# Kernel tuning notes

Hardware: AMD Instinct MI355X
Metric: run time of the kernel (lower is better)

Reference implementation:

```python
import jax, jax.numpy as jnp
import numpy as np

N, F_IN, H1, C1, C2, Q, E = 50000, 256, 4, 32, 128, 768, 800000
NEG_SLOPE = 0.2


def gat_layer(x, src, dst, W, a_src, a_dst, bias, heads, ch, num_nodes):
    # x: [N, F]; W: [F, heads*ch]; a_src/a_dst: [heads, ch]
    xw = (x @ W).reshape(num_nodes, heads, ch)
    alpha_s = jnp.sum(xw * a_src, axis=-1)  # [N, heads]
    alpha_d = jnp.sum(xw * a_dst, axis=-1)  # [N, heads]
    e = jax.nn.leaky_relu(alpha_s[src] + alpha_d[dst], NEG_SLOPE)  # [E, heads]
    # segment softmax over destination nodes (every node has a self-loop)
    m = jax.ops.segment_max(e, dst, num_segments=num_nodes)
    e = jnp.exp(e - m[dst])
    denom = jax.ops.segment_sum(e, dst, num_segments=num_nodes)
    alpha = e / (denom[dst] + 1e-16)  # [E, heads]
    msg = alpha[:, :, None] * xw[src]  # [E, heads, ch]
    out = jax.ops.segment_sum(msg, dst, num_segments=num_nodes)
    return out.reshape(num_nodes, heads * ch) + bias


def setup_inputs() -> dict:
    key = jax.random.key(0)
    ks = jax.random.split(key, 16)
    s = lambda fan_in: 1.0 / np.sqrt(fan_in)
    return {
        "entity_features": jax.random.normal(ks[0], (N, F_IN), jnp.float32),
        "edge_index": jax.random.randint(ks[1], (2, E), 0, N, jnp.int32),
        "question_embedding": jax.random.normal(ks[2], (Q,), jnp.float32),
        "question_entity_mask": jax.random.randint(ks[3], (N,), 0, 2, jnp.int32),
        "place_entity_mask": jax.random.randint(ks[4], (N,), 0, 2, jnp.int32),
        "W1": jax.random.normal(ks[5], (F_IN, H1 * C1), jnp.float32) * s(F_IN),
        "att_src1": jax.random.normal(ks[6], (H1, C1), jnp.float32) * s(C1),
        "att_dst1": jax.random.normal(ks[7], (H1, C1), jnp.float32) * s(C1),
        "b1": jnp.zeros((H1 * C1,), jnp.float32),
        "W2": jax.random.normal(ks[8], (H1 * C1, C2), jnp.float32) * s(H1 * C1),
        "att_src2": jax.random.normal(ks[9], (1, C2), jnp.float32) * s(C2),
        "att_dst2": jax.random.normal(ks[10], (1, C2), jnp.float32) * s(C2),
        "b2": jnp.zeros((C2,), jnp.float32),
        "Wq": jax.random.normal(ks[11], (C2 + Q, 1), jnp.float32) * s(C2 + Q),
        "bq": jnp.zeros((1,), jnp.float32),
    }


def reference(entity_features, edge_index, question_embedding, question_entity_mask,
              place_entity_mask, W1, att_src1, att_dst1, b1, W2, att_src2, att_dst2, b2, Wq, bq):
    # add self-loops (PyG GATConv default add_self_loops=True)
    loops = jnp.arange(N, dtype=edge_index.dtype)
    src = jnp.concatenate([edge_index[0], loops])
    dst = jnp.concatenate([edge_index[1], loops])

    x = gat_layer(entity_features, src, dst, W1, att_src1, att_dst1, b1, H1, C1, N)
    x = jax.nn.elu(x)  # dropout is identity in eval
    ents = gat_layer(x, src, dst, W2, att_src2, att_dst2, b2, 1, C2, N)
    ents = jax.nn.elu(ents)  # [N, C2]

    q = jnp.broadcast_to(question_embedding[None, :], (N, Q))
    combined = jnp.concatenate([ents, q], axis=-1)  # [N, C2+Q]
    logits = (combined @ Wq + bq)[:, 0]  # [N]
    logits = logits + (question_entity_mask.astype(jnp.float32) - 1.0) * 1e9
    attn = jax.nn.softmax(logits, axis=0)  # [N]
    pooled = jnp.sum(attn[:, None] * ents, axis=0)  # [C2]
    return pooled, ents, attn
```

## Files before the change

### kernel.cpp

```cpp
#include <hip/hip_runtime.h>
#include <hip/hip_fp16.h>
#include <math.h>

#define N_NODES 50000
#define F_IN    256
#define H1      4
#define C1      32
#define HC      128
#define C2      128
#define QDIM    768
#define NE      800000
#define NB_SCAN 196
#define NB_POOL 512


__device__ __forceinline__ void atomicMaxFloat(float* addr, float val) {
    if (val >= 0.f)
        atomicMax(reinterpret_cast<int*>(addr), __float_as_int(val));
    else
        atomicMin(reinterpret_cast<unsigned int*>(addr), __float_as_uint(val));
}


__global__ void init_scal_kernel(float* scal) {
    scal[1] = -INFINITY;
    scal[2] = 0.f;
}

__global__ void qdot_kernel(const float* __restrict__ q, const float* __restrict__ Wq,
                            const float* __restrict__ bq, float* scal) {
    __shared__ float sm[256];
    float acc = 0.f;
    for (int i = threadIdx.x; i < QDIM; i += 256) acc += q[i] * Wq[C2 + i];
    sm[threadIdx.x] = acc;
    __syncthreads();
    for (int o = 128; o > 0; o >>= 1) {
        if (threadIdx.x < o) sm[threadIdx.x] += sm[threadIdx.x + o];
        __syncthreads();
    }
    if (threadIdx.x == 0) scal[0] = sm[0] + bq[0];
}


__global__ void hist_kernel(const int* __restrict__ ei, int* __restrict__ deg) {
    int e = blockIdx.x * blockDim.x + threadIdx.x;
    if (e >= NE) return;
    atomicAdd(&deg[ei[NE + e]], 1);
}

__global__ void scan1_kernel(const int* __restrict__ deg, int* __restrict__ incl,
                             int* __restrict__ bsum) {
    __shared__ int sm[256];
    int i = blockIdx.x * 256 + threadIdx.x;
    int v = (i < N_NODES) ? deg[i] : 0;
    sm[threadIdx.x] = v;
    __syncthreads();
    for (int o = 1; o < 256; o <<= 1) {
        int t = (threadIdx.x >= o) ? sm[threadIdx.x - o] : 0;
        __syncthreads();
        sm[threadIdx.x] += t;
        __syncthreads();
    }
    if (i < N_NODES) incl[i] = sm[threadIdx.x];
    if (threadIdx.x == 255) bsum[blockIdx.x] = sm[255];
}

__global__ void scan2_kernel(int* __restrict__ bsum) {
    __shared__ int sm[256];
    int v = (threadIdx.x < NB_SCAN) ? bsum[threadIdx.x] : 0;
    sm[threadIdx.x] = v;
    __syncthreads();
    for (int o = 1; o < 256; o <<= 1) {
        int t = (threadIdx.x >= o) ? sm[threadIdx.x - o] : 0;
        __syncthreads();
        sm[threadIdx.x] += t;
        __syncthreads();
    }
    if (threadIdx.x < NB_SCAN) bsum[threadIdx.x] = sm[threadIdx.x] - v;
}

__global__ void scan3_kernel(const int* __restrict__ deg, const int* __restrict__ incl,
                             const int* __restrict__ bsum, int* __restrict__ rowptr,
                             int* __restrict__ cursor) {
    int i = blockIdx.x * 256 + threadIdx.x;
    if (i >= N_NODES) return;
    int excl = incl[i] - deg[i] + bsum[i >> 8];
    rowptr[i] = excl;
    cursor[i] = excl;
    if (i == N_NODES - 1) rowptr[N_NODES] = excl + deg[i];
}

__global__ void scatter_kernel(const int* __restrict__ ei, int* __restrict__ cursor,
                               int* __restrict__ colsrc) {
    int e = blockIdx.x * blockDim.x + threadIdx.x;
    if (e >= NE) return;
    int s = ei[e], d = ei[NE + e];
    int pos = atomicAdd(&cursor[d], 1);
    colsrc[pos] = s;
}


#define BM 64
#define BN 128
#define BKK 16

__global__ __launch_bounds__(256) void gemm_f32(const float* __restrict__ A,
                                                const float* __restrict__ B,
                                                __half* __restrict__ Ch,
                                                int M, int K) {
    __shared__ float As[BKK][BM + 4];
    __shared__ float Bs[BKK][BN];
    const int t  = threadIdx.x;
    const int tx = t & 15, ty = t >> 4;
    const int row0 = blockIdx.x * BM;

    const int ar  = t >> 2;
    const int akb = (t & 3) * 4;
    const int bk = t >> 5;
    const int bn = (t * 4) & 127;

    float acc[4][8] = {};

    for (int k0 = 0; k0 < K; k0 += BKK) {
        float4 av = make_float4(0.f, 0.f, 0.f, 0.f);
        if (row0 + ar < M)
            av = *reinterpret_cast<const float4*>(A + (long)(row0 + ar) * K + k0 + akb);
        As[akb + 0][ar] = av.x;
        As[akb + 1][ar] = av.y;
        As[akb + 2][ar] = av.z;
        As[akb + 3][ar] = av.w;
        *reinterpret_cast<float4*>(&Bs[bk][bn]) =
            *reinterpret_cast<const float4*>(B + (long)(k0 + bk) * BN + bn);
        *reinterpret_cast<float4*>(&Bs[bk + 8][bn]) =
            *reinterpret_cast<const float4*>(B + (long)(k0 + bk + 8) * BN + bn);
        __syncthreads();
#pragma unroll
        for (int k = 0; k < BKK; k++) {
            float4 a  = *reinterpret_cast<const float4*>(&As[k][ty * 4]);
            float4 b0 = *reinterpret_cast<const float4*>(&Bs[k][tx * 4]);
            float4 b1 = *reinterpret_cast<const float4*>(&Bs[k][64 + tx * 4]);
            float aa[4] = {a.x, a.y, a.z, a.w};
            float bb[8] = {b0.x, b0.y, b0.z, b0.w, b1.x, b1.y, b1.z, b1.w};
#pragma unroll
            for (int i = 0; i < 4; i++)
#pragma unroll
                for (int j = 0; j < 8; j++) acc[i][j] += aa[i] * bb[j];
        }
        __syncthreads();
    }
#pragma unroll
    for (int i = 0; i < 4; i++) {
        int r = row0 + ty * 4 + i;
        if (r < M) {
            union { __half2 h2[2]; uint2 u; } p0, p1;
            p0.h2[0] = __floats2half2_rn(acc[i][0], acc[i][1]);
            p0.h2[1] = __floats2half2_rn(acc[i][2], acc[i][3]);
            p1.h2[0] = __floats2half2_rn(acc[i][4], acc[i][5]);
            p1.h2[1] = __floats2half2_rn(acc[i][6], acc[i][7]);
            *reinterpret_cast<uint2*>(Ch + (long)r * BN + tx * 4)      = p0.u;
            *reinterpret_cast<uint2*>(Ch + (long)r * BN + 64 + tx * 4) = p1.u;
        }
    }
}


__global__ void alpha_kernel(const __half* __restrict__ xw,
                             const float* __restrict__ a_src,
                             const float* __restrict__ a_dst,
                             float* __restrict__ as_, float* __restrict__ ad_,
                             int NH, int H, int C) {
    int i = blockIdx.x * blockDim.x + threadIdx.x;
    if (i >= NH) return;
    int n = i / H, h = i - n * H;
    const __half2* row = reinterpret_cast<const __half2*>(xw + (long)n * HC + h * C);
    const float* vs  = a_src + h * C;
    const float* vd  = a_dst + h * C;
    float s = 0.f, d = 0.f;
    for (int k2 = 0; k2 < C / 2; k2++) {
        float2 f = __half22float2(row[k2]);
        s += f.x * vs[2 * k2] + f.y * vs[2 * k2 + 1];
        d += f.x * vd[2 * k2] + f.y * vd[2 * k2 + 1];
    }
    as_[i] = s;
    ad_[i] = d;
}


template<int H>
__global__ __launch_bounds__(256) void gat_agg_kernel(const int* __restrict__ rowptr,
                                                      const int* __restrict__ colsrc,
                                                      const float* __restrict__ as_,
                                                      const float* __restrict__ ad_,
                                                      const __half* __restrict__ xw,
                                                      const float* __restrict__ bias,
                                                      float* __restrict__ outbuf,
                                                      int fuse_elu) {
    constexpr int CHUNK = 64 / H;
    int n    = (blockIdx.x * blockDim.x + threadIdx.x) >> 6;
    int lane = threadIdx.x & 63;
    if (n >= N_NODES) return;
    const int c     = lane * 2;
    const int h_my  = lane / CHUNK;
    const int eslot = lane & (CHUNK - 1);
    const int gbase = lane - eslot;

    const float adn = ad_[n * H + h_my];
    float m;
    {
        float v = as_[n * H + h_my] + adn;
        m = (v > 0.f) ? v : 0.2f * v;
    }
    float den = 1.f;
    float2 acc = __half22float2(*reinterpret_cast<const __half2*>(xw + (long)n * HC + c));

    const int rbeg = rowptr[n], rend = rowptr[n + 1];
    for (int base = rbeg; base < rend; base += CHUNK) {
        int idx = base + eslot;
        int s   = (idx < rend) ? colsrc[idx] : -1;
        float ev;
        if (s >= 0) {
            float v = as_[(long)s * H + h_my] + adn;
            ev = (v > 0.f) ? v : 0.2f * v;
        } else {
            ev = -INFINITY;
        }
        float cm = ev;
#pragma unroll
        for (int o = CHUNK / 2; o > 0; o >>= 1) cm = fmaxf(cm, __shfl_xor(cm, o));
        float nm = fmaxf(m, cm);
        float sc = __expf(m - nm);
        den *= sc;
        acc.x *= sc; acc.y *= sc;
        m = nm;
        float e_ = (s >= 0) ? __expf(ev - nm) : 0.f;
        float ssum = e_;
#pragma unroll
        for (int o = CHUNK / 2; o > 0; o >>= 1) ssum += __shfl_xor(ssum, o);
        den += ssum;
        int cnt = min(CHUNK, rend - base);
#pragma unroll 4
        for (int j = 0; j < cnt; j++) {
            int   sj = __shfl(s, j);
            float aj = __shfl(e_, gbase + j);
            const float2 v =
                __half22float2(*reinterpret_cast<const __half2*>(xw + (long)sj * HC + c));
            acc.x += aj * v.x;
            acc.y += aj * v.y;
        }
    }

    float inv = 1.f / (den + 1e-16f);
    float x0 = acc.x * inv, x1 = acc.y * inv;
    if (fuse_elu) {
        x0 += bias[c]; x1 += bias[c + 1];
        x0 = (x0 > 0.f) ? x0 : (__expf(x0) - 1.f);
        x1 = (x1 > 0.f) ? x1 : (__expf(x1) - 1.f);
    }
    float2 o; o.x = x0; o.y = x1;
    *reinterpret_cast<float2*>(outbuf + (long)n * HC + c) = o;
}


__global__ __launch_bounds__(256) void ents_logits_kernel(float* __restrict__ ents,
                                                          const float* __restrict__ b2,
                                                          const float* __restrict__ Wq,
                                                          const int* __restrict__ qmask,
                                                          const float* __restrict__ scal,
                                                          float* __restrict__ logits) {
    int wid  = (blockIdx.x * blockDim.x + threadIdx.x) >> 6;
    int lane = threadIdx.x & 63;
    if (wid >= N_NODES) return;
    int c = lane * 2;
    float2 v = *reinterpret_cast<float2*>(ents + (long)wid * HC + c);
    float x0 = v.x + b2[c], x1 = v.y + b2[c + 1];
    x0 = (x0 > 0.f) ? x0 : (__expf(x0) - 1.f);
    x1 = (x1 > 0.f) ? x1 : (__expf(x1) - 1.f);
    float2 w; w.x = x0; w.y = x1;
    *reinterpret_cast<float2*>(ents + (long)wid * HC + c) = w;
    float acc = x0 * Wq[c] + x1 * Wq[c + 1];
#pragma unroll
    for (int o = 32; o > 0; o >>= 1) acc += __shfl_down(acc, o);
    if (lane == 0)
        logits[wid] = acc + scal[0] + ((float)qmask[wid] - 1.f) * 1e9f;
}

__global__ __launch_bounds__(256) void red_max_kernel(const float* __restrict__ logits,
                                                      float* scal) {
    __shared__ float sm[256];
    float mx = -INFINITY;
    for (int i = blockIdx.x * 256 + threadIdx.x; i < N_NODES; i += gridDim.x * 256)
        mx = fmaxf(mx, logits[i]);
    sm[threadIdx.x] = mx;
    __syncthreads();
    for (int o = 128; o > 0; o >>= 1) {
        if (threadIdx.x < o) sm[threadIdx.x] = fmaxf(sm[threadIdx.x], sm[threadIdx.x + o]);
        __syncthreads();
    }
    if (threadIdx.x == 0) atomicMaxFloat(&scal[1], sm[0]);
}

__global__ __launch_bounds__(256) void red_sum_kernel(float* __restrict__ logits,
                                                      float* scal) {
    __shared__ float sm[256];
    const float gmax = scal[1];
    float acc = 0.f;
    for (int i = blockIdx.x * 256 + threadIdx.x; i < N_NODES; i += gridDim.x * 256) {
        float ex = __expf(logits[i] - gmax);
        logits[i] = ex;
        acc += ex;
    }
    sm[threadIdx.x] = acc;
    __syncthreads();
    for (int o = 128; o > 0; o >>= 1) {
        if (threadIdx.x < o) sm[threadIdx.x] += sm[threadIdx.x + o];
        __syncthreads();
    }
    if (threadIdx.x == 0) unsafeAtomicAdd(&scal[2], sm[0]);
}

__global__ void attn_kernel(const float* __restrict__ logits, const float* __restrict__ scal,
                            float* __restrict__ attn_out) {
    int n = blockIdx.x * blockDim.x + threadIdx.x;
    if (n >= N_NODES) return;
    attn_out[n] = logits[n] / scal[2];
}

__global__ __launch_bounds__(128) void pooled_partial_kernel(const float* __restrict__ ents,
                                                             const float* __restrict__ attn,
                                                             float* __restrict__ partial) {
    int c = threadIdx.x;
    float acc = 0.f;
    for (int n = blockIdx.x; n < N_NODES; n += gridDim.x)
        acc += attn[n] * ents[(long)n * HC + c];
    partial[(long)blockIdx.x * HC + c] = acc;
}

__global__ __launch_bounds__(128) void pooled_reduce_kernel(const float* __restrict__ partial,
                                                            float* __restrict__ pooled) {
    int c = threadIdx.x;
    float acc = 0.f;
    for (int b = 0; b < NB_POOL; b++) acc += partial[(long)b * HC + c];
    pooled[c] = acc;
}


extern "C" void kernel_launch(void* const* d_in, const int* in_sizes, int n_in,
                              void* d_out, int out_size, void* d_ws, size_t ws_size,
                              hipStream_t stream) {
    const float* x     = (const float*)d_in[0];
    const int*   ei    = (const int*)d_in[1];
    const float* q     = (const float*)d_in[2];
    const int*   qmask = (const int*)d_in[3];
    const float* W1    = (const float*)d_in[5];
    const float* asrc1 = (const float*)d_in[6];
    const float* adst1 = (const float*)d_in[7];
    const float* b1    = (const float*)d_in[8];
    const float* W2    = (const float*)d_in[9];
    const float* asrc2 = (const float*)d_in[10];
    const float* adst2 = (const float*)d_in[11];
    const float* b2    = (const float*)d_in[12];
    const float* Wq    = (const float*)d_in[13];
    const float* bq    = (const float*)d_in[14];

    float* out    = (float*)d_out;
    float* pooled = out;
    float* ents   = out + HC;
    float* attn   = out + HC + (long)N_NODES * HC;

    float*  ws     = (float*)d_ws;
    __half* xw     = (__half*)ws;
    float* as1     = ws + (long)N_NODES * HC / 2;
    float* ad1     = as1 + N_NODES * H1;
    float* as2     = ad1 + N_NODES * H1;
    float* ad2     = as2 + N_NODES;
    float* logits  = ad2 + N_NODES;
    float* scal    = logits + N_NODES;
    float* partial = scal + 4;
    int*   deg     = (int*)(partial + NB_POOL * HC);
    int*   incl    = deg + N_NODES;
    int*   bsum    = incl + N_NODES;
    int*   rowptr  = bsum + 256;
    int*   cursor  = rowptr + N_NODES + 1;
    int*   colsrc  = cursor + N_NODES;

    const int TB = 256;
    const int g_nh1 = (N_NODES * H1 + TB - 1) / TB;
    const int g_n   = (N_NODES + TB - 1) / TB;
    const int g_e   = (NE + TB - 1) / TB;
    const int g_nw  = (N_NODES + 3) / 4;
    const int g_gemm = (N_NODES + BM - 1) / BM;

    hipMemsetAsync(deg, 0, N_NODES * sizeof(int), stream);
    init_scal_kernel<<<1, 1, 0, stream>>>(scal);
    qdot_kernel<<<1, TB, 0, stream>>>(q, Wq, bq, scal);

    hist_kernel<<<g_e, TB, 0, stream>>>(ei, deg);
    scan1_kernel<<<NB_SCAN, TB, 0, stream>>>(deg, incl, bsum);
    scan2_kernel<<<1, TB, 0, stream>>>(bsum);
    scan3_kernel<<<NB_SCAN, TB, 0, stream>>>(deg, incl, bsum, rowptr, cursor);
    scatter_kernel<<<g_e, TB, 0, stream>>>(ei, cursor, colsrc);

    gemm_f32<<<g_gemm, TB, 0, stream>>>(x, W1, xw, N_NODES, F_IN);
    alpha_kernel<<<g_nh1, TB, 0, stream>>>(xw, asrc1, adst1, as1, ad1, N_NODES * H1, H1, C1);
    gat_agg_kernel<H1><<<g_nw, TB, 0, stream>>>(rowptr, colsrc, as1, ad1, xw, b1, ents, 1);

    gemm_f32<<<g_gemm, TB, 0, stream>>>(ents, W2, xw, N_NODES, HC);
    alpha_kernel<<<g_n, TB, 0, stream>>>(xw, asrc2, adst2, as2, ad2, N_NODES, 1, C2);
    gat_agg_kernel<1><<<g_nw, TB, 0, stream>>>(rowptr, colsrc, as2, ad2, xw, b2, ents, 0);

    ents_logits_kernel<<<g_nw, TB, 0, stream>>>(ents, b2, Wq, qmask, scal, logits);
    red_max_kernel<<<NB_SCAN, TB, 0, stream>>>(logits, scal);
    red_sum_kernel<<<NB_SCAN, TB, 0, stream>>>(logits, scal);
    attn_kernel<<<g_n, TB, 0, stream>>>(logits, scal, attn);
    pooled_partial_kernel<<<NB_POOL, 128, 0, stream>>>(ents, attn, partial);
    pooled_reduce_kernel<<<1, 128, 0, stream>>>(partial, pooled);
}
```

Before: 511.8 us.

## Gather 16-byte fp16 rows, four edges per wavefront in GAT aggregation

Each wavefront now splits into four 16-lane groups, and each group handles a different neighbor edge. Every lane loads 8 fp16 channels through a 16-byte vector load instead of 2 channels through a 4-byte load. Partial accumulators are combined with cross-group shuffles at the end, and only group 0 writes the result with float4 stores. This is meant to cut the number of serial gather iterations and widen the memory transactions, at the cost of more registers, extra shuffles, and padded loads clamped to row 0 when the edge count is not a multiple of 4.

```diff
diff --git a/kernel.cpp b/kernel.cpp
--- a/kernel.cpp
+++ b/kernel.cpp
@@ -199,10 +199,12 @@
     int n    = (blockIdx.x * blockDim.x + threadIdx.x) >> 6;
     int lane = threadIdx.x & 63;
     if (n >= N_NODES) return;
-    const int c     = lane * 2;
     const int h_my  = lane / CHUNK;
     const int eslot = lane & (CHUNK - 1);
-    const int gbase = lane - eslot;
+    const int l16   = lane & 15;
+    const int grp   = lane >> 4;
+    const int cbase = l16 * 8;
+    const int hg    = (H == 1) ? 0 : (cbase >> 5);
 
     const float adn = ad_[n * H + h_my];
     float m;
@@ -211,7 +213,18 @@
         m = (v > 0.f) ? v : 0.2f * v;
     }
     float den = 1.f;
-    float2 acc = __half22float2(*reinterpret_cast<const __half2*>(xw + (long)n * HC + c));
+
+    float acc[8] = {};
+    if (grp == 0) {
+        union { uint4 u; __half2 h[4]; } cv;
+        cv.u = *reinterpret_cast<const uint4*>(xw + (long)n * HC + cbase);
+#pragma unroll
+        for (int k = 0; k < 4; k++) {
+            float2 f = __half22float2(cv.h[k]);
+            acc[2 * k]     = f.x;
+            acc[2 * k + 1] = f.y;
+        }
+    }
 
     const int rbeg = rowptr[n], rend = rowptr[n + 1];
     for (int base = rbeg; base < rend; base += CHUNK) {
@@ -230,34 +243,56 @@
         float nm = fmaxf(m, cm);
         float sc = __expf(m - nm);
         den *= sc;
-        acc.x *= sc; acc.y *= sc;
         m = nm;
         float e_ = (s >= 0) ? __expf(ev - nm) : 0.f;
         float ssum = e_;
 #pragma unroll
         for (int o = CHUNK / 2; o > 0; o >>= 1) ssum += __shfl_xor(ssum, o);
         den += ssum;
+        float sc_g = (H == 1) ? sc : __shfl(sc, hg * CHUNK);
+#pragma unroll
+        for (int k = 0; k < 8; k++) acc[k] *= sc_g;
         int cnt = min(CHUNK, rend - base);
 #pragma unroll 4
-        for (int j = 0; j < cnt; j++) {
-            int   sj = __shfl(s, j);
-            float aj = __shfl(e_, gbase + j);
-            const float2 v =
-                __half22float2(*reinterpret_cast<const __half2*>(xw + (long)sj * HC + c));
-            acc.x += aj * v.x;
-            acc.y += aj * v.y;
-        }
-    }
-
-    float inv = 1.f / (den + 1e-16f);
-    float x0 = acc.x * inv, x1 = acc.y * inv;
-    if (fuse_elu) {
-        x0 += bias[c]; x1 += bias[c + 1];
-        x0 = (x0 > 0.f) ? x0 : (__expf(x0) - 1.f);
-        x1 = (x1 > 0.f) ? x1 : (__expf(x1) - 1.f);
-    }
-    float2 o; o.x = x0; o.y = x1;
-    *reinterpret_cast<float2*>(outbuf + (long)n * HC + c) = o;
+        for (int j4 = 0; j4 < cnt; j4 += 4) {
+            int eidx = j4 + grp;
+            int   sj = __shfl(s,  eidx);
+            float aj = __shfl(e_, hg * CHUNK + eidx);
+            int  sjc = (sj < 0) ? 0 : sj;
+            union { uint4 u; __half2 h[4]; } cv;
+            cv.u = *reinterpret_cast<const uint4*>(xw + (long)sjc * HC + cbase);
+#pragma unroll
+            for (int k = 0; k < 4; k++) {
+                float2 f = __half22float2(cv.h[k]);
+                acc[2 * k]     += aj * f.x;
+                acc[2 * k + 1] += aj * f.y;
+            }
+        }
+    }
+
+#pragma unroll
+    for (int k = 0; k < 8; k++) {
+        acc[k] += __shfl_xor(acc[k], 16);
+        acc[k] += __shfl_xor(acc[k], 32);
+    }
+    float den_g = (H == 1) ? den : __shfl(den, hg * CHUNK);
+    if (grp == 0) {
+        float inv = 1.f / (den_g + 1e-16f);
+        float o[8];
+#pragma unroll
+        for (int k = 0; k < 8; k++) {
+            float v = acc[k] * inv;
+            if (fuse_elu) {
+                v += bias[cbase + k];
+                v = (v > 0.f) ? v : (__expf(v) - 1.f);
+            }
+            o[k] = v;
+        }
+        float4 o0 = make_float4(o[0], o[1], o[2], o[3]);
+        float4 o1 = make_float4(o[4], o[5], o[6], o[7]);
+        *reinterpret_cast<float4*>(outbuf + (long)n * HC + cbase)     = o0;
+        *reinterpret_cast<float4*>(outbuf + (long)n * HC + cbase + 4) = o1;
+    }
 }
 
 
```

New measurement: 482.4 us. -5.7%, faster.
